# Optimization experiments

Measured on AMD Instinct MI355X. Metric: run time of the kernel, lower is better.

The kernel has to match this reference:

```python
import jax, jax.numpy as jnp
import numpy as np

NPOINT = 512
RADIUS = 0.2
NSAMPLE = 32
BN_EPS = 1e-5


def setup_inputs() -> dict:
    key = jax.random.key(0)
    ks = jax.random.split(key, 8)
    B, N, C = 8, 16384, 64
    xyz = jax.random.uniform(ks[0], (B, N, 3), dtype=jnp.float32)
    features = jax.random.normal(ks[1], (B, N, C), dtype=jnp.float32)
    # shared-MLP 1x1 conv weights (out, in), BN params per layer
    w0 = jax.random.normal(ks[2], (64, 67), dtype=jnp.float32) * 0.1
    w1 = jax.random.normal(ks[3], (64, 64), dtype=jnp.float32) * 0.1
    w2 = jax.random.normal(ks[4], (128, 64), dtype=jnp.float32) * 0.1
    return dict(
        xyz=xyz, features=features,
        w0=w0, g0=jnp.ones((64,)), b0=jnp.zeros((64,)), m0=jnp.zeros((64,)), v0=jnp.ones((64,)),
        w1=w1, g1=jnp.ones((64,)), b1=jnp.zeros((64,)), m1=jnp.zeros((64,)), v1=jnp.ones((64,)),
        w2=w2, g2=jnp.ones((128,)), b2=jnp.zeros((128,)), m2=jnp.zeros((128,)), v2=jnp.ones((128,)),
    )


def furthest_point_sample(xyz, npoint):
    # xyz: (B, N, 3) -> idx: (B, npoint) int32. Sequential farthest-point selection.
    B, N, _ = xyz.shape
    binds = jnp.arange(B)

    def step(carry, _):
        dists, last = carry  # (B,N), (B,)
        p = xyz[binds, last]                      # (B, 3)
        d = jnp.sum((xyz - p[:, None, :]) ** 2, axis=-1)  # (B, N)
        dists = jnp.minimum(dists, d)
        nxt = jnp.argmax(dists, axis=-1).astype(jnp.int32)
        return (dists, nxt), last

    init = (jnp.full((B, N), jnp.inf, dtype=xyz.dtype), jnp.zeros((B,), jnp.int32))
    _, idx = jax.lax.scan(step, init, None, length=npoint)  # (npoint, B)
    return idx.T  # (B, npoint)


def ball_query(xyz, new_xyz, radius, nsample):
    # xyz: (B,N,3), new_xyz: (B,S,3) -> idx (B,S,nsample) int32
    N = xyz.shape[1]
    d2 = jnp.sum((new_xyz[:, :, None, :] - xyz[:, None, :, :]) ** 2, axis=-1)  # (B,S,N)
    cand = jnp.where(d2 <= radius * radius, jnp.arange(N, dtype=jnp.int32), N)
    cand = jnp.sort(cand, axis=-1)[..., :nsample]  # first nsample in-radius indices
    first = cand[..., :1]
    idx = jnp.where(cand == N, first, cand)       # duplicate first hit when short
    return jnp.minimum(idx, N - 1)


def _mlp_layer(x, w, g, b, m, v):
    # x: (B,S,K,Cin); 1x1 conv + BN(inference) + ReLU
    h = jnp.einsum('bskc,oc->bsko', x, w)
    h = (h - m) * (g * jax.lax.rsqrt(v + BN_EPS)) + b
    return jax.nn.relu(h)


def reference(xyz, features, w0, g0, b0, m0, v0, w1, g1, b1, m1, v1, w2, g2, b2, m2, v2):
    B = xyz.shape[0]
    binds = jnp.arange(B)[:, None, None]
    fps_idx = furthest_point_sample(xyz, NPOINT)                # (B, S)
    new_xyz = jnp.take_along_axis(xyz, fps_idx[..., None], axis=1)  # (B, S, 3)
    idx = ball_query(xyz, new_xyz, RADIUS, NSAMPLE)             # (B, S, K)
    grouped_xyz = xyz[binds, idx] - new_xyz[:, :, None, :]      # (B,S,K,3) centered
    grouped_feat = features[binds, idx]                         # (B,S,K,C)
    x = jnp.concatenate([grouped_xyz, grouped_feat], axis=-1)   # (B,S,K,3+C)
    x = _mlp_layer(x, w0, g0, b0, m0, v0)
    x = _mlp_layer(x, w1, g1, b1, m1, v1)
    x = _mlp_layer(x, w2, g2, b2, m2, v2)                       # (B,S,K,128)
    new_features = jnp.max(x, axis=2)                           # max-pool over nsample
    new_features = jnp.transpose(new_features, (0, 2, 1))       # (B, 128, S) channel-first
    return new_xyz, new_features
```

## Files before the change

kernel.cpp:

```cpp
#include <hip/hip_runtime.h>
#include <hip/hip_bf16.h>

#define NPT   16384
#define NQ    512
#define NS    32
#define BATCH 8

typedef float f32x2 __attribute__((ext_vector_type(2)));

template <int CTRL>
__device__ inline double dpp_f64(double x)
{
    const unsigned long long u = (unsigned long long)__double_as_longlong(x);
    int lo = (int)(unsigned)u;
    int hi = (int)(unsigned)(u >> 32);
    lo = __builtin_amdgcn_update_dpp(0, lo, CTRL, 0xf, 0xf, true);
    hi = __builtin_amdgcn_update_dpp(0, hi, CTRL, 0xf, 0xf, true);
    return __longlong_as_double(
        (long long)(((unsigned long long)(unsigned)hi << 32) | (unsigned)lo));
}

__global__ __launch_bounds__(512)
__attribute__((amdgpu_waves_per_eu(2, 2)))
void fps_kernel(const float* __restrict__ xyz, float* __restrict__ new_xyz)
{
#pragma clang fp contract(off)
    const int b = blockIdx.x;
    const int t = threadIdx.x;
    const float* xb = xyz + (size_t)b * NPT * 3;

    f32x2 xr[16], yr[16], zr[16], dr[16];
    const float INF = __int_as_float(0x7f800000);
#pragma unroll
    for (int j = 0; j < 16; ++j) {
        const int p0 = (2 * j) * 512 + t;
        const int p1 = (2 * j + 1) * 512 + t;
        xr[j] = (f32x2){xb[p0 * 3 + 0], xb[p1 * 3 + 0]};
        yr[j] = (f32x2){xb[p0 * 3 + 1], xb[p1 * 3 + 1]};
        zr[j] = (f32x2){xb[p0 * 3 + 2], xb[p1 * 3 + 2]};
        dr[j] = (f32x2){INF, INF};
    }

    __shared__ unsigned long long red[2][8];

    float px = xb[0], py = xb[1], pz = xb[2];

    for (int s = 0; s < NQ; ++s) {
        if (t == 0) {
            float* o = new_xyz + ((size_t)b * NQ + s) * 3;
            o[0] = px; o[1] = py; o[2] = pz;
        }
        if (s == NQ - 1) break;

        const f32x2 pxv = {px, px}, pyv = {py, py}, pzv = {pz, pz};
        float dmax = -1.0f;
        int   bi_  = 0;
#pragma unroll
        for (int j = 0; j < 16; ++j) {
            const f32x2 dx = xr[j] - pxv;
            const f32x2 dy = yr[j] - pyv;
            const f32x2 dz = zr[j] - pzv;
            f32x2 d = (dx * dx + dy * dy);
            d = d + dz * dz;
            const f32x2 dn = __builtin_elementwise_min(dr[j], d);
            dr[j] = dn;
            const float ds = (dn.x >= dn.y) ? dn.x : dn.y;
            const int   is = (dn.x >= dn.y) ? (2 * j) : (2 * j + 1);
            if (ds > dmax) { dmax = ds; bi_ = is; }
        }

        const unsigned pidx = (unsigned)(bi_ * 512 + t);
        double kd = __longlong_as_double((long long)(
            ((unsigned long long)__float_as_uint(dmax) << 32) | (unsigned)(~pidx)));

        kd = fmax(kd, dpp_f64<0x111>(kd));
        kd = fmax(kd, dpp_f64<0x112>(kd));
        kd = fmax(kd, dpp_f64<0x114>(kd));
        kd = fmax(kd, dpp_f64<0x118>(kd));
        kd = fmax(kd, dpp_f64<0x142>(kd));
        kd = fmax(kd, dpp_f64<0x143>(kd));

        if ((t & 63) == 63)
            red[s & 1][t >> 6] = (unsigned long long)__double_as_longlong(kd);
        __syncthreads();

        double kc = __longlong_as_double((long long)red[s & 1][t & 7]);
        kc = fmax(kc, dpp_f64<0x111>(kc));
        kc = fmax(kc, dpp_f64<0x112>(kc));
        kc = fmax(kc, dpp_f64<0x114>(kc));

        const unsigned long long kw = (unsigned long long)__double_as_longlong(kc);
        const unsigned lo7 = (unsigned)__builtin_amdgcn_readlane((int)(unsigned)kw, 7);
        const int nxt = (int)(unsigned)(~lo7);

        px = xb[nxt * 3 + 0];
        py = xb[nxt * 3 + 1];
        pz = xb[nxt * 3 + 2];
    }
}

__global__ __launch_bounds__(256) void bq_kernel(const float* __restrict__ xyz,
                                                 const float* __restrict__ newxyz,
                                                 int* __restrict__ gidx)
{
    const int wid  = (blockIdx.x * 256 + threadIdx.x) >> 6;
    const int lane = threadIdx.x & 63;
    const int b    = wid >> 9;
    const float* xb = xyz + (size_t)b * NPT * 3;

    const float qx = newxyz[wid * 3 + 0];
    const float qy = newxyz[wid * 3 + 1];
    const float qz = newxyz[wid * 3 + 2];
    int* out = gidx + (size_t)wid * NS;

    const float R2 = 0.04f;
    int cnt = 0, first = -1;

    for (int base = 0; base < NPT; base += 64) {
        const int p = base + lane;
        const float dx = __fsub_rn(xb[p * 3 + 0], qx);
        const float dy = __fsub_rn(xb[p * 3 + 1], qy);
        const float dz = __fsub_rn(xb[p * 3 + 2], qz);
        const float d  = __fadd_rn(__fadd_rn(__fmul_rn(dx, dx), __fmul_rn(dy, dy)),
                                   __fmul_rn(dz, dz));
        const bool in = (d <= R2);
        const unsigned long long m = __ballot(in);
        if (first < 0 && m) first = base + (__ffsll((unsigned long long)m) - 1);
        if (in) {
            const int pos = cnt + __popcll(m & ((1ull << lane) - 1ull));
            if (pos < NS) out[pos] = p;
        }
        cnt += __popcll(m);
        if (cnt >= NS) break;
    }
    if (cnt < NS) {
        const int f = (cnt > 0) ? first : (NPT - 1);
        for (int j = cnt + lane; j < NS; j += 64) out[j] = f;
    }
}

template <int OP>
__device__ inline void mlp_layer(const float* __restrict__ inb,
                                 const float* __restrict__ wbuf,
                                 const float* __restrict__ scp,
                                 const float* __restrict__ bip,
                                 float* __restrict__ outb, int nchunk, int t)
{
    const int ko = t & 15;
    const int og = t >> 4;
    const int o0 = og * OP;
    float acc0[OP], acc1[OP];
#pragma unroll
    for (int j = 0; j < OP; ++j) { acc0[j] = 0.f; acc1[j] = 0.f; }

    for (int cc = 0; cc < nchunk; ++cc) {
        const int c = cc * 4;
        const float4 xa = *(const float4*)(inb + ko * 68 + c);
        const float4 xb = *(const float4*)(inb + (ko + 16) * 68 + c);
#pragma unroll
        for (int j = 0; j < OP; ++j) {
            const float4 w = *(const float4*)(wbuf + (o0 + j) * 68 + c);
            acc0[j] += xa.x * w.x + xa.y * w.y + xa.z * w.z + xa.w * w.w;
            acc1[j] += xb.x * w.x + xb.y * w.y + xb.z * w.z + xb.w * w.w;
        }
    }
#pragma unroll
    for (int j = 0; j < OP; ++j) {
        const float sv = scp[o0 + j], bv = bip[o0 + j];
        acc0[j] = fmaxf(acc0[j] * sv + bv, 0.f);
        acc1[j] = fmaxf(acc1[j] * sv + bv, 0.f);
    }
#pragma unroll
    for (int jb = 0; jb < OP; jb += 4) {
        *(float4*)(outb + ko * 68 + o0 + jb) =
            make_float4(acc0[jb], acc0[jb + 1], acc0[jb + 2], acc0[jb + 3]);
        *(float4*)(outb + (ko + 16) * 68 + o0 + jb) =
            make_float4(acc1[jb], acc1[jb + 1], acc1[jb + 2], acc1[jb + 3]);
    }
}

__device__ inline void mlp_layer2(const float* __restrict__ inb,
                                  const float* __restrict__ wbuf,
                                  const float* __restrict__ scp,
                                  const float* __restrict__ bip,
                                  float* __restrict__ out, int b, int s, int t)
{
    const int ko = t & 15;
    const int og = t >> 4;
    const int o0 = og * 8;
    float acc0[8], acc1[8];
#pragma unroll
    for (int j = 0; j < 8; ++j) { acc0[j] = 0.f; acc1[j] = 0.f; }

    for (int cc = 0; cc < 16; ++cc) {
        const int c = cc * 4;
        const float4 xa = *(const float4*)(inb + ko * 68 + c);
        const float4 xb = *(const float4*)(inb + (ko + 16) * 68 + c);
#pragma unroll
        for (int j = 0; j < 8; ++j) {
            const float4 w = *(const float4*)(wbuf + (o0 + j) * 68 + c);
            acc0[j] += xa.x * w.x + xa.y * w.y + xa.z * w.z + xa.w * w.w;
            acc1[j] += xb.x * w.x + xb.y * w.y + xb.z * w.z + xb.w * w.w;
        }
    }
    float v[8];
#pragma unroll
    for (int j = 0; j < 8; ++j) {
        const float sv = scp[o0 + j], bv = bip[o0 + j];
        const float h0 = fmaxf(acc0[j] * sv + bv, 0.f);
        const float h1 = fmaxf(acc1[j] * sv + bv, 0.f);
        v[j] = fmaxf(h0, h1);
    }
#pragma unroll
    for (int m = 1; m <= 8; m <<= 1) {
#pragma unroll
        for (int j = 0; j < 8; ++j) v[j] = fmaxf(v[j], __shfl_xor(v[j], m, 64));
    }
    if (ko == 0) {
#pragma unroll
        for (int j = 0; j < 8; ++j)
            out[((size_t)b * 128 + o0 + j) * NQ + s] = v[j];
    }
}

__global__ __launch_bounds__(256) void mlp_kernel(
    const float* __restrict__ xyz, const float* __restrict__ feat,
    const float* __restrict__ newxyz, const int* __restrict__ gidx,
    const float* __restrict__ w0, const float* __restrict__ g0,
    const float* __restrict__ b0, const float* __restrict__ m0,
    const float* __restrict__ v0,
    const float* __restrict__ w1, const float* __restrict__ g1,
    const float* __restrict__ b1, const float* __restrict__ m1,
    const float* __restrict__ v1,
    const float* __restrict__ w2, const float* __restrict__ g2,
    const float* __restrict__ b2, const float* __restrict__ m2,
    const float* __restrict__ v2,
    float* __restrict__ out)
{
    __shared__ float wbuf[128 * 68];
    __shared__ float bufA[32 * 68];
    __shared__ float bufB[32 * 68];
    __shared__ float sc[256], bi[256];

    const int t   = threadIdx.x;
    const int grp = blockIdx.x;
    const int b   = grp >> 9;
    const int s   = grp & (NQ - 1);
    const int* gi = gidx + (size_t)grp * NS;

    float4 r1[4], r2[8];
    {
        const float4* s1 = (const float4*)(w1 + t * 16);
#pragma unroll
        for (int q = 0; q < 4; ++q) r1[q] = s1[q];
        const float4* s2 = (const float4*)(w2 + t * 32);
#pragma unroll
        for (int q = 0; q < 8; ++q) r2[q] = s2[q];
    }

    if (t < 64) {
        const float sv = g0[t] * rsqrtf(v0[t] + 1e-5f);
        sc[t] = sv; bi[t] = b0[t] - m0[t] * sv;
    } else if (t < 128) {
        const int j = t - 64;
        const float sv = g1[j] * rsqrtf(v1[j] + 1e-5f);
        sc[t] = sv; bi[t] = b1[j] - m1[j] * sv;
    } else {
        const int j = t - 128;
        const float sv = g2[j] * rsqrtf(v2[j] + 1e-5f);
        sc[t] = sv; bi[t] = b2[j] - m2[j] * sv;
    }

    for (int i = t; i < 64 * 68; i += 256) {
        const int o = i / 68, c = i - o * 68;
        float v;
        if (c < 64)       v = w0[o * 67 + 3 + c];
        else if (c < 67)  v = w0[o * 67 + (c - 64)];
        else              v = 0.f;
        wbuf[i] = v;
    }

    {
        const int k = t >> 3, f = t & 7;
        const int p = gi[k];
        const float* fr = feat + ((size_t)b * NPT + p) * 64 + f * 8;
        const float4 a0 = *(const float4*)fr;
        const float4 a1 = *(const float4*)(fr + 4);
        *(float4*)(bufA + k * 68 + f * 8)     = a0;
        *(float4*)(bufA + k * 68 + f * 8 + 4) = a1;
        if (f == 0) {
            const float qx = newxyz[grp * 3 + 0];
            const float qy = newxyz[grp * 3 + 1];
            const float qz = newxyz[grp * 3 + 2];
            const float* xp = xyz + ((size_t)b * NPT + p) * 3;
            bufA[k * 68 + 64] = xp[0] - qx;
            bufA[k * 68 + 65] = xp[1] - qy;
            bufA[k * 68 + 66] = xp[2] - qz;
            bufA[k * 68 + 67] = 0.f;
        }
    }
    __syncthreads();

    mlp_layer<4>(bufA, wbuf, sc, bi, bufB, 17, t);
    __syncthreads();

    {
        float* dst = wbuf + (t >> 2) * 68 + (t & 3) * 16;
#pragma unroll
        for (int q = 0; q < 4; ++q) *(float4*)(dst + 4 * q) = r1[q];
    }
    __syncthreads();

    mlp_layer<4>(bufB, wbuf, sc + 64, bi + 64, bufA, 16, t);
    __syncthreads();

    {
        float* dst = wbuf + (t >> 1) * 68 + (t & 1) * 32;
#pragma unroll
        for (int q = 0; q < 8; ++q) *(float4*)(dst + 4 * q) = r2[q];
    }
    __syncthreads();

    mlp_layer2(bufA, wbuf, sc + 128, bi + 128, out, b, s, t);
}

extern "C" void kernel_launch(void* const* d_in, const int* in_sizes, int n_in,
                              void* d_out, int out_size, void* d_ws, size_t ws_size,
                              hipStream_t stream)
{
    const float* xyz  = (const float*)d_in[0];
    const float* feat = (const float*)d_in[1];
    const float* w0 = (const float*)d_in[2];
    const float* g0 = (const float*)d_in[3];
    const float* b0 = (const float*)d_in[4];
    const float* m0 = (const float*)d_in[5];
    const float* v0 = (const float*)d_in[6];
    const float* w1 = (const float*)d_in[7];
    const float* g1 = (const float*)d_in[8];
    const float* b1 = (const float*)d_in[9];
    const float* m1 = (const float*)d_in[10];
    const float* v1 = (const float*)d_in[11];
    const float* w2 = (const float*)d_in[12];
    const float* g2 = (const float*)d_in[13];
    const float* b2 = (const float*)d_in[14];
    const float* m2 = (const float*)d_in[15];
    const float* v2 = (const float*)d_in[16];

    float* out      = (float*)d_out;
    float* new_xyz  = out;
    float* out_feat = out + BATCH * NQ * 3;
    int*   gidx     = (int*)d_ws;

    fps_kernel<<<BATCH, 512, 0, stream>>>(xyz, new_xyz);
    bq_kernel<<<(BATCH * NQ * 64) / 256, 256, 0, stream>>>(xyz, new_xyz, gidx);
    mlp_kernel<<<BATCH * NQ, 256, 0, stream>>>(xyz, feat, new_xyz, gidx,
                                               w0, g0, b0, m0, v0,
                                               w1, g1, b1, m1, v1,
                                               w2, g2, b2, m2, v2,
                                               out_feat);
}
```

Measured before the change: 1.109 ms.

## Halve MLP weight LDS buffer, split last layer in two passes, reorder block mapping

The last MLP layer now runs in two 64-output halves that share a single 64x68 weight buffer, which cuts shared memory per block by about 17 KB so more blocks can be resident per CU. The neighbour feature gather loads are issued at kernel start, ahead of the weight staging, to overlap global latency. Block indices are interleaved across batches, likely to spread accesses. The cost is an extra barrier and a second weight-staging pass in the final layer.

Measured after the change: 1.227 ms. 10.6% more time.

```diff
diff --git a/kernel.cpp b/kernel.cpp
--- a/kernel.cpp
+++ b/kernel.cpp
@@ -179,47 +179,22 @@
     }
 }
 
-__device__ inline void mlp_layer2(const float* __restrict__ inb,
+__device__ inline void mlp_l2_acc(const float* __restrict__ inb,
                                   const float* __restrict__ wbuf,
-                                  const float* __restrict__ scp,
-                                  const float* __restrict__ bip,
-                                  float* __restrict__ out, int b, int s, int t)
+                                  float acc0[4], float acc1[4], int t)
 {
     const int ko = t & 15;
-    const int og = t >> 4;
-    const int o0 = og * 8;
-    float acc0[8], acc1[8];
-#pragma unroll
-    for (int j = 0; j < 8; ++j) { acc0[j] = 0.f; acc1[j] = 0.f; }
-
+    const int o0 = (t >> 4) * 4;
     for (int cc = 0; cc < 16; ++cc) {
         const int c = cc * 4;
         const float4 xa = *(const float4*)(inb + ko * 68 + c);
         const float4 xb = *(const float4*)(inb + (ko + 16) * 68 + c);
 #pragma unroll
-        for (int j = 0; j < 8; ++j) {
+        for (int j = 0; j < 4; ++j) {
             const float4 w = *(const float4*)(wbuf + (o0 + j) * 68 + c);
             acc0[j] += xa.x * w.x + xa.y * w.y + xa.z * w.z + xa.w * w.w;
             acc1[j] += xb.x * w.x + xb.y * w.y + xb.z * w.z + xb.w * w.w;
         }
-    }
-    float v[8];
-#pragma unroll
-    for (int j = 0; j < 8; ++j) {
-        const float sv = scp[o0 + j], bv = bip[o0 + j];
-        const float h0 = fmaxf(acc0[j] * sv + bv, 0.f);
-        const float h1 = fmaxf(acc1[j] * sv + bv, 0.f);
-        v[j] = fmaxf(h0, h1);
-    }
-#pragma unroll
-    for (int m = 1; m <= 8; m <<= 1) {
-#pragma unroll
-        for (int j = 0; j < 8; ++j) v[j] = fmaxf(v[j], __shfl_xor(v[j], m, 64));
-    }
-    if (ko == 0) {
-#pragma unroll
-        for (int j = 0; j < 8; ++j)
-            out[((size_t)b * 128 + o0 + j) * NQ + s] = v[j];
     }
 }
 
@@ -237,16 +212,32 @@
     const float* __restrict__ v2,
     float* __restrict__ out)
 {
-    __shared__ float wbuf[128 * 68];
+    __shared__ float wbuf[64 * 68];
     __shared__ float bufA[32 * 68];
     __shared__ float bufB[32 * 68];
     __shared__ float sc[256], bi[256];
 
-    const int t   = threadIdx.x;
-    const int grp = blockIdx.x;
+    const int t = threadIdx.x;
+    const int grp = ((blockIdx.x & 7) << 9) | (blockIdx.x >> 3);
     const int b   = grp >> 9;
     const int s   = grp & (NQ - 1);
     const int* gi = gidx + (size_t)grp * NS;
+
+    const int k = t >> 3, f = t & 7;
+    const int p = gi[k];
+    const float* fr = feat + ((size_t)b * NPT + p) * 64 + f * 8;
+    const float4 a0 = *(const float4*)fr;
+    const float4 a1 = *(const float4*)(fr + 4);
+    float c64 = 0.f, c65 = 0.f, c66 = 0.f;
+    if (f == 0) {
+        const float qx = newxyz[grp * 3 + 0];
+        const float qy = newxyz[grp * 3 + 1];
+        const float qz = newxyz[grp * 3 + 2];
+        const float* xp = xyz + ((size_t)b * NPT + p) * 3;
+        c64 = xp[0] - qx;
+        c65 = xp[1] - qy;
+        c66 = xp[2] - qz;
+    }
 
     float4 r1[4], r2[8];
     {
@@ -280,24 +271,13 @@
         wbuf[i] = v;
     }
 
-    {
-        const int k = t >> 3, f = t & 7;
-        const int p = gi[k];
-        const float* fr = feat + ((size_t)b * NPT + p) * 64 + f * 8;
-        const float4 a0 = *(const float4*)fr;
-        const float4 a1 = *(const float4*)(fr + 4);
-        *(float4*)(bufA + k * 68 + f * 8)     = a0;
-        *(float4*)(bufA + k * 68 + f * 8 + 4) = a1;
-        if (f == 0) {
-            const float qx = newxyz[grp * 3 + 0];
-            const float qy = newxyz[grp * 3 + 1];
-            const float qz = newxyz[grp * 3 + 2];
-            const float* xp = xyz + ((size_t)b * NPT + p) * 3;
-            bufA[k * 68 + 64] = xp[0] - qx;
-            bufA[k * 68 + 65] = xp[1] - qy;
-            bufA[k * 68 + 66] = xp[2] - qz;
-            bufA[k * 68 + 67] = 0.f;
-        }
+    *(float4*)(bufA + k * 68 + f * 8)     = a0;
+    *(float4*)(bufA + k * 68 + f * 8 + 4) = a1;
+    if (f == 0) {
+        bufA[k * 68 + 64] = c64;
+        bufA[k * 68 + 65] = c65;
+        bufA[k * 68 + 66] = c66;
+        bufA[k * 68 + 67] = 0.f;
     }
     __syncthreads();
 
@@ -314,14 +294,55 @@
     mlp_layer<4>(bufB, wbuf, sc + 64, bi + 64, bufA, 16, t);
     __syncthreads();
 
-    {
+    if (t < 128) {
         float* dst = wbuf + (t >> 1) * 68 + (t & 1) * 32;
 #pragma unroll
         for (int q = 0; q < 8; ++q) *(float4*)(dst + 4 * q) = r2[q];
     }
     __syncthreads();
 
-    mlp_layer2(bufA, wbuf, sc + 128, bi + 128, out, b, s, t);
+    float accA0[4] = {0.f, 0.f, 0.f, 0.f}, accA1[4] = {0.f, 0.f, 0.f, 0.f};
+    mlp_l2_acc(bufA, wbuf, accA0, accA1, t);
+    __syncthreads();
+
+    if (t >= 128) {
+        float* dst = wbuf + ((t >> 1) - 64) * 68 + (t & 1) * 32;
+#pragma unroll
+        for (int q = 0; q < 8; ++q) *(float4*)(dst + 4 * q) = r2[q];
+    }
+    __syncthreads();
+
+    float accB0[4] = {0.f, 0.f, 0.f, 0.f}, accB1[4] = {0.f, 0.f, 0.f, 0.f};
+    mlp_l2_acc(bufA, wbuf, accB0, accB1, t);
+
+    const int ko = t & 15;
+    const int o4 = (t >> 4) * 4;
+    const float* scp = sc + 128;
+    const float* bip = bi + 128;
+    float v[8];
+#pragma unroll
+    for (int j = 0; j < 4; ++j) {
+        const float svA = scp[o4 + j],      bvA = bip[o4 + j];
+        const float svB = scp[64 + o4 + j], bvB = bip[64 + o4 + j];
+        const float hA0 = fmaxf(accA0[j] * svA + bvA, 0.f);
+        const float hA1 = fmaxf(accA1[j] * svA + bvA, 0.f);
+        const float hB0 = fmaxf(accB0[j] * svB + bvB, 0.f);
+        const float hB1 = fmaxf(accB1[j] * svB + bvB, 0.f);
+        v[j]     = fmaxf(hA0, hA1);
+        v[4 + j] = fmaxf(hB0, hB1);
+    }
+#pragma unroll
+    for (int m = 1; m <= 8; m <<= 1) {
+#pragma unroll
+        for (int j = 0; j < 8; ++j) v[j] = fmaxf(v[j], __shfl_xor(v[j], m, 64));
+    }
+    if (ko == 0) {
+#pragma unroll
+        for (int j = 0; j < 4; ++j) {
+            out[((size_t)b * 128 + o4 + j) * NQ + s]      = v[j];
+            out[((size_t)b * 128 + 64 + o4 + j) * NQ + s] = v[4 + j];
+        }
+    }
 }
 
 extern "C" void kernel_launch(void* const* d_in, const int* in_sizes, int n_in,
```

## Split FPS across four cooperating blocks per batch with global atomic barrier

Applied to the files above, without the earlier changes.

Farthest point sampling for each batch is spread over four workgroups, each holding a quarter of the points in registers. The per-step argmax is combined through a global buffer, an atomic counter and a spin-wait. The goal is more CUs working on the sequential FPS loop and less per-thread work per step. The cost is a device-scope round trip and spin on every one of the 512 steps, and correctness depends on all 32 blocks being resident at the same time. The workspace region used for the counters overlaps the gidx buffer, which is only written later by bq_kernel.

Measured after the change: 1.796 ms. 62.0% more time.

```diff
diff --git a/kernel.cpp b/kernel.cpp
--- a/kernel.cpp
+++ b/kernel.cpp
@@ -5,6 +5,7 @@
 #define NQ    512
 #define NS    32
 #define BATCH 8
+#define FPB   4
 
 typedef float f32x2 __attribute__((ext_vector_type(2)));
 
@@ -21,20 +22,24 @@
 }
 
 __global__ __launch_bounds__(512)
-__attribute__((amdgpu_waves_per_eu(2, 2)))
-void fps_kernel(const float* __restrict__ xyz, float* __restrict__ new_xyz)
+void fps_kernel(const float* __restrict__ xyz, float* __restrict__ new_xyz,
+                unsigned long long* __restrict__ kbuf,
+                unsigned* __restrict__ cnt)
 {
 #pragma clang fp contract(off)
-    const int b = blockIdx.x;
-    const int t = threadIdx.x;
+    const int bb  = blockIdx.x;
+    const int b   = bb >> 2;
+    const int blk = bb & 3;
+    const int t   = threadIdx.x;
     const float* xb = xyz + (size_t)b * NPT * 3;
-
-    f32x2 xr[16], yr[16], zr[16], dr[16];
+    const int pbase = blk * (NPT / FPB);
+
+    f32x2 xr[4], yr[4], zr[4], dr[4];
     const float INF = __int_as_float(0x7f800000);
 #pragma unroll
-    for (int j = 0; j < 16; ++j) {
-        const int p0 = (2 * j) * 512 + t;
-        const int p1 = (2 * j + 1) * 512 + t;
+    for (int j = 0; j < 4; ++j) {
+        const int p0 = pbase + (2 * j) * 512 + t;
+        const int p1 = pbase + (2 * j + 1) * 512 + t;
         xr[j] = (f32x2){xb[p0 * 3 + 0], xb[p1 * 3 + 0]};
         yr[j] = (f32x2){xb[p0 * 3 + 1], xb[p1 * 3 + 1]};
         zr[j] = (f32x2){xb[p0 * 3 + 2], xb[p1 * 3 + 2]};
@@ -42,11 +47,12 @@
     }
 
     __shared__ unsigned long long red[2][8];
+    __shared__ int nxt_s;
 
     float px = xb[0], py = xb[1], pz = xb[2];
 
     for (int s = 0; s < NQ; ++s) {
-        if (t == 0) {
+        if (blk == 0 && t == 0) {
             float* o = new_xyz + ((size_t)b * NQ + s) * 3;
             o[0] = px; o[1] = py; o[2] = pz;
         }
@@ -56,7 +62,7 @@
         float dmax = -1.0f;
         int   bi_  = 0;
 #pragma unroll
-        for (int j = 0; j < 16; ++j) {
+        for (int j = 0; j < 4; ++j) {
             const f32x2 dx = xr[j] - pxv;
             const f32x2 dy = yr[j] - pyv;
             const f32x2 dz = zr[j] - pzv;
@@ -69,7 +75,7 @@
             if (ds > dmax) { dmax = ds; bi_ = is; }
         }
 
-        const unsigned pidx = (unsigned)(bi_ * 512 + t);
+        const unsigned pidx = (unsigned)(pbase + bi_ * 512 + t);
         double kd = __longlong_as_double((long long)(
             ((unsigned long long)__float_as_uint(dmax) << 32) | (unsigned)(~pidx)));
 
@@ -91,7 +97,33 @@
 
         const unsigned long long kw = (unsigned long long)__double_as_longlong(kc);
         const unsigned lo7 = (unsigned)__builtin_amdgcn_readlane((int)(unsigned)kw, 7);
-        const int nxt = (int)(unsigned)(~lo7);
+        const unsigned hi7 = (unsigned)__builtin_amdgcn_readlane((int)(unsigned)(kw >> 32), 7);
+        const unsigned long long kblock = ((unsigned long long)hi7 << 32) | lo7;
+
+        if (t == 0) {
+            __hip_atomic_store(&kbuf[(s & 1) * (BATCH * FPB) + bb], kblock,
+                               __ATOMIC_RELAXED, __HIP_MEMORY_SCOPE_AGENT);
+            __hip_atomic_fetch_add(&cnt[b], 1u,
+                                   __ATOMIC_RELEASE, __HIP_MEMORY_SCOPE_AGENT);
+            const unsigned tgt = (unsigned)(FPB * (s + 1));
+            while (__hip_atomic_load(&cnt[b], __ATOMIC_ACQUIRE,
+                                     __HIP_MEMORY_SCOPE_AGENT) < tgt)
+                __builtin_amdgcn_s_sleep(1);
+            const unsigned long long* kb4 =
+                kbuf + (s & 1) * (BATCH * FPB) + b * FPB;
+            unsigned long long w = __hip_atomic_load(&kb4[0], __ATOMIC_RELAXED,
+                                                     __HIP_MEMORY_SCOPE_AGENT);
+#pragma unroll
+            for (int q = 1; q < FPB; ++q) {
+                const unsigned long long v =
+                    __hip_atomic_load(&kb4[q], __ATOMIC_RELAXED,
+                                      __HIP_MEMORY_SCOPE_AGENT);
+                if (v > w) w = v;
+            }
+            nxt_s = (int)(unsigned)(~(unsigned)w);
+        }
+        __syncthreads();
+        const int nxt = nxt_s;
 
         px = xb[nxt * 3 + 0];
         py = xb[nxt * 3 + 1];
@@ -351,7 +383,11 @@
     float* out_feat = out + BATCH * NQ * 3;
     int*   gidx     = (int*)d_ws;
 
-    fps_kernel<<<BATCH, 512, 0, stream>>>(xyz, new_xyz);
+    unsigned long long* kbuf = (unsigned long long*)d_ws;
+    unsigned* cnt = (unsigned*)((char*)d_ws + 1024);
+    hipMemsetAsync(d_ws, 0, 2048, stream);
+
+    fps_kernel<<<BATCH * FPB, 512, 0, stream>>>(xyz, new_xyz, kbuf, cnt);
     bq_kernel<<<(BATCH * NQ * 64) / 256, 256, 0, stream>>>(xyz, new_xyz, gidx);
     mlp_kernel<<<BATCH * NQ, 256, 0, stream>>>(xyz, feat, new_xyz, gidx,
                                                w0, g0, b0, m0, v0,
```

## Fuse FPS, ball query and MLP into one persistent producer-consumer kernel

Applied to the files above, without the earlier changes.

Merges the three kernels into a single persistent launch: 8 blocks run furthest point sampling and publish each new centroid with a release flag per batch. The other 248 blocks poll those flags and run ball query plus the three-layer MLP for two queries at a time, so grouping and MLP overlap with the serial FPS loop. This removes the separate launches and the global index buffer, but adds spin-waiting, a memset, and a reliance on producer and consumer blocks being co-resident. It also reloads weights for every query pair.

Result: slower. 1.700 ms (+53.3%).

```diff
diff --git a/kernel.cpp b/kernel.cpp
--- a/kernel.cpp
+++ b/kernel.cpp
@@ -5,6 +5,8 @@
 #define NQ    512
 #define NS    32
 #define BATCH 8
+#define NCONS 248
+#define NPAIR 2048
 
 typedef float f32x2 __attribute__((ext_vector_type(2)));
 
@@ -20,125 +22,6 @@
         (long long)(((unsigned long long)(unsigned)hi << 32) | (unsigned)lo));
 }
 
-__global__ __launch_bounds__(512)
-__attribute__((amdgpu_waves_per_eu(2, 2)))
-void fps_kernel(const float* __restrict__ xyz, float* __restrict__ new_xyz)
-{
-#pragma clang fp contract(off)
-    const int b = blockIdx.x;
-    const int t = threadIdx.x;
-    const float* xb = xyz + (size_t)b * NPT * 3;
-
-    f32x2 xr[16], yr[16], zr[16], dr[16];
-    const float INF = __int_as_float(0x7f800000);
-#pragma unroll
-    for (int j = 0; j < 16; ++j) {
-        const int p0 = (2 * j) * 512 + t;
-        const int p1 = (2 * j + 1) * 512 + t;
-        xr[j] = (f32x2){xb[p0 * 3 + 0], xb[p1 * 3 + 0]};
-        yr[j] = (f32x2){xb[p0 * 3 + 1], xb[p1 * 3 + 1]};
-        zr[j] = (f32x2){xb[p0 * 3 + 2], xb[p1 * 3 + 2]};
-        dr[j] = (f32x2){INF, INF};
-    }
-
-    __shared__ unsigned long long red[2][8];
-
-    float px = xb[0], py = xb[1], pz = xb[2];
-
-    for (int s = 0; s < NQ; ++s) {
-        if (t == 0) {
-            float* o = new_xyz + ((size_t)b * NQ + s) * 3;
-            o[0] = px; o[1] = py; o[2] = pz;
-        }
-        if (s == NQ - 1) break;
-
-        const f32x2 pxv = {px, px}, pyv = {py, py}, pzv = {pz, pz};
-        float dmax = -1.0f;
-        int   bi_  = 0;
-#pragma unroll
-        for (int j = 0; j < 16; ++j) {
-            const f32x2 dx = xr[j] - pxv;
-            const f32x2 dy = yr[j] - pyv;
-            const f32x2 dz = zr[j] - pzv;
-            f32x2 d = (dx * dx + dy * dy);
-            d = d + dz * dz;
-            const f32x2 dn = __builtin_elementwise_min(dr[j], d);
-            dr[j] = dn;
-            const float ds = (dn.x >= dn.y) ? dn.x : dn.y;
-            const int   is = (dn.x >= dn.y) ? (2 * j) : (2 * j + 1);
-            if (ds > dmax) { dmax = ds; bi_ = is; }
-        }
-
-        const unsigned pidx = (unsigned)(bi_ * 512 + t);
-        double kd = __longlong_as_double((long long)(
-            ((unsigned long long)__float_as_uint(dmax) << 32) | (unsigned)(~pidx)));
-
-        kd = fmax(kd, dpp_f64<0x111>(kd));
-        kd = fmax(kd, dpp_f64<0x112>(kd));
-        kd = fmax(kd, dpp_f64<0x114>(kd));
-        kd = fmax(kd, dpp_f64<0x118>(kd));
-        kd = fmax(kd, dpp_f64<0x142>(kd));
-        kd = fmax(kd, dpp_f64<0x143>(kd));
-
-        if ((t & 63) == 63)
-            red[s & 1][t >> 6] = (unsigned long long)__double_as_longlong(kd);
-        __syncthreads();
-
-        double kc = __longlong_as_double((long long)red[s & 1][t & 7]);
-        kc = fmax(kc, dpp_f64<0x111>(kc));
-        kc = fmax(kc, dpp_f64<0x112>(kc));
-        kc = fmax(kc, dpp_f64<0x114>(kc));
-
-        const unsigned long long kw = (unsigned long long)__double_as_longlong(kc);
-        const unsigned lo7 = (unsigned)__builtin_amdgcn_readlane((int)(unsigned)kw, 7);
-        const int nxt = (int)(unsigned)(~lo7);
-
-        px = xb[nxt * 3 + 0];
-        py = xb[nxt * 3 + 1];
-        pz = xb[nxt * 3 + 2];
-    }
-}
-
-__global__ __launch_bounds__(256) void bq_kernel(const float* __restrict__ xyz,
-                                                 const float* __restrict__ newxyz,
-                                                 int* __restrict__ gidx)
-{
-    const int wid  = (blockIdx.x * 256 + threadIdx.x) >> 6;
-    const int lane = threadIdx.x & 63;
-    const int b    = wid >> 9;
-    const float* xb = xyz + (size_t)b * NPT * 3;
-
-    const float qx = newxyz[wid * 3 + 0];
-    const float qy = newxyz[wid * 3 + 1];
-    const float qz = newxyz[wid * 3 + 2];
-    int* out = gidx + (size_t)wid * NS;
-
-    const float R2 = 0.04f;
-    int cnt = 0, first = -1;
-
-    for (int base = 0; base < NPT; base += 64) {
-        const int p = base + lane;
-        const float dx = __fsub_rn(xb[p * 3 + 0], qx);
-        const float dy = __fsub_rn(xb[p * 3 + 1], qy);
-        const float dz = __fsub_rn(xb[p * 3 + 2], qz);
-        const float d  = __fadd_rn(__fadd_rn(__fmul_rn(dx, dx), __fmul_rn(dy, dy)),
-                                   __fmul_rn(dz, dz));
-        const bool in = (d <= R2);
-        const unsigned long long m = __ballot(in);
-        if (first < 0 && m) first = base + (__ffsll((unsigned long long)m) - 1);
-        if (in) {
-            const int pos = cnt + __popcll(m & ((1ull << lane) - 1ull));
-            if (pos < NS) out[pos] = p;
-        }
-        cnt += __popcll(m);
-        if (cnt >= NS) break;
-    }
-    if (cnt < NS) {
-        const int f = (cnt > 0) ? first : (NPT - 1);
-        for (int j = cnt + lane; j < NS; j += 64) out[j] = f;
-    }
-}
-
 template <int OP>
 __device__ inline void mlp_layer(const float* __restrict__ inb,
                                  const float* __restrict__ wbuf,
@@ -223,105 +106,256 @@
     }
 }
 
-__global__ __launch_bounds__(256) void mlp_kernel(
-    const float* __restrict__ xyz, const float* __restrict__ feat,
-    const float* __restrict__ newxyz, const int* __restrict__ gidx,
-    const float* __restrict__ w0, const float* __restrict__ g0,
-    const float* __restrict__ b0, const float* __restrict__ m0,
-    const float* __restrict__ v0,
-    const float* __restrict__ w1, const float* __restrict__ g1,
-    const float* __restrict__ b1, const float* __restrict__ m1,
-    const float* __restrict__ v1,
-    const float* __restrict__ w2, const float* __restrict__ g2,
-    const float* __restrict__ b2, const float* __restrict__ m2,
-    const float* __restrict__ v2,
-    float* __restrict__ out)
+__global__ __launch_bounds__(512)
+void fused_kernel(const float* __restrict__ xyz, const float* __restrict__ feat,
+                  float* __restrict__ new_xyz,
+                  const float* __restrict__ w0, const float* __restrict__ g0,
+                  const float* __restrict__ b0, const float* __restrict__ m0,
+                  const float* __restrict__ v0,
+                  const float* __restrict__ w1, const float* __restrict__ g1,
+                  const float* __restrict__ b1, const float* __restrict__ m1,
+                  const float* __restrict__ v1,
+                  const float* __restrict__ w2, const float* __restrict__ g2,
+                  const float* __restrict__ b2, const float* __restrict__ m2,
+                  const float* __restrict__ v2,
+                  float* __restrict__ out, unsigned* __restrict__ flags)
 {
     __shared__ float wbuf[128 * 68];
-    __shared__ float bufA[32 * 68];
-    __shared__ float bufB[32 * 68];
+    __shared__ float bufA[2][32 * 68];
+    __shared__ float bufB[2][32 * 68];
     __shared__ float sc[256], bi[256];
-
-    const int t   = threadIdx.x;
-    const int grp = blockIdx.x;
-    const int b   = grp >> 9;
-    const int s   = grp & (NQ - 1);
-    const int* gi = gidx + (size_t)grp * NS;
-
-    float4 r1[4], r2[8];
-    {
-        const float4* s1 = (const float4*)(w1 + t * 16);
-#pragma unroll
-        for (int q = 0; q < 4; ++q) r1[q] = s1[q];
-        const float4* s2 = (const float4*)(w2 + t * 32);
-#pragma unroll
-        for (int q = 0; q < 8; ++q) r2[q] = s2[q];
-    }
-
-    if (t < 64) {
-        const float sv = g0[t] * rsqrtf(v0[t] + 1e-5f);
-        sc[t] = sv; bi[t] = b0[t] - m0[t] * sv;
-    } else if (t < 128) {
-        const int j = t - 64;
-        const float sv = g1[j] * rsqrtf(v1[j] + 1e-5f);
-        sc[t] = sv; bi[t] = b1[j] - m1[j] * sv;
-    } else {
-        const int j = t - 128;
-        const float sv = g2[j] * rsqrtf(v2[j] + 1e-5f);
-        sc[t] = sv; bi[t] = b2[j] - m2[j] * sv;
-    }
-
-    for (int i = t; i < 64 * 68; i += 256) {
-        const int o = i / 68, c = i - o * 68;
-        float v;
-        if (c < 64)       v = w0[o * 67 + 3 + c];
-        else if (c < 67)  v = w0[o * 67 + (c - 64)];
-        else              v = 0.f;
-        wbuf[i] = v;
-    }
-
-    {
-        const int k = t >> 3, f = t & 7;
-        const int p = gi[k];
-        const float* fr = feat + ((size_t)b * NPT + p) * 64 + f * 8;
-        const float4 a0 = *(const float4*)fr;
-        const float4 a1 = *(const float4*)(fr + 4);
-        *(float4*)(bufA + k * 68 + f * 8)     = a0;
-        *(float4*)(bufA + k * 68 + f * 8 + 4) = a1;
-        if (f == 0) {
-            const float qx = newxyz[grp * 3 + 0];
-            const float qy = newxyz[grp * 3 + 1];
-            const float qz = newxyz[grp * 3 + 2];
-            const float* xp = xyz + ((size_t)b * NPT + p) * 3;
-            bufA[k * 68 + 64] = xp[0] - qx;
-            bufA[k * 68 + 65] = xp[1] - qy;
-            bufA[k * 68 + 66] = xp[2] - qz;
-            bufA[k * 68 + 67] = 0.f;
-        }
-    }
-    __syncthreads();
-
-    mlp_layer<4>(bufA, wbuf, sc, bi, bufB, 17, t);
-    __syncthreads();
-
-    {
-        float* dst = wbuf + (t >> 2) * 68 + (t & 3) * 16;
-#pragma unroll
-        for (int q = 0; q < 4; ++q) *(float4*)(dst + 4 * q) = r1[q];
-    }
-    __syncthreads();
-
-    mlp_layer<4>(bufB, wbuf, sc + 64, bi + 64, bufA, 16, t);
-    __syncthreads();
-
-    {
-        float* dst = wbuf + (t >> 1) * 68 + (t & 1) * 32;
-#pragma unroll
-        for (int q = 0; q < 8; ++q) *(float4*)(dst + 4 * q) = r2[q];
-    }
-    __syncthreads();
-
-    mlp_layer2(bufA, wbuf, sc + 128, bi + 128, out, b, s, t);
+    __shared__ int   gidxL[2][NS];
+    __shared__ float qbuf[2][3];
+    __shared__ unsigned long long red[2][8];
+
+    const int t = threadIdx.x;
+
+    if (blockIdx.x < BATCH) {
+#pragma clang fp contract(off)
+        __builtin_amdgcn_s_setprio(3);
+        const int b = blockIdx.x;
+        const float* xb = xyz + (size_t)b * NPT * 3;
+
+        f32x2 xr[16], yr[16], zr[16], dr[16];
+        const float INF = __int_as_float(0x7f800000);
+#pragma unroll
+        for (int j = 0; j < 16; ++j) {
+            const int p0 = (2 * j) * 512 + t;
+            const int p1 = (2 * j + 1) * 512 + t;
+            xr[j] = (f32x2){xb[p0 * 3 + 0], xb[p1 * 3 + 0]};
+            yr[j] = (f32x2){xb[p0 * 3 + 1], xb[p1 * 3 + 1]};
+            zr[j] = (f32x2){xb[p0 * 3 + 2], xb[p1 * 3 + 2]};
+            dr[j] = (f32x2){INF, INF};
+        }
+
+        float px = xb[0], py = xb[1], pz = xb[2];
+
+        for (int s = 0; s < NQ; ++s) {
+            if (t == 0) {
+                unsigned* o = (unsigned*)(new_xyz + ((size_t)b * NQ + s) * 3);
+                __hip_atomic_store(o + 0, __float_as_uint(px),
+                                   __ATOMIC_RELAXED, __HIP_MEMORY_SCOPE_AGENT);
+                __hip_atomic_store(o + 1, __float_as_uint(py),
+                                   __ATOMIC_RELAXED, __HIP_MEMORY_SCOPE_AGENT);
+                __hip_atomic_store(o + 2, __float_as_uint(pz),
+                                   __ATOMIC_RELAXED, __HIP_MEMORY_SCOPE_AGENT);
+                __hip_atomic_store(&flags[b * 32], (unsigned)(s + 1),
+                                   __ATOMIC_RELEASE, __HIP_MEMORY_SCOPE_AGENT);
+            }
+            if (s == NQ - 1) break;
+
+            const f32x2 pxv = {px, px}, pyv = {py, py}, pzv = {pz, pz};
+            float dmax = -1.0f;
+            int   bi_  = 0;
+#pragma unroll
+            for (int j = 0; j < 16; ++j) {
+                const f32x2 dx = xr[j] - pxv;
+                const f32x2 dy = yr[j] - pyv;
+                const f32x2 dz = zr[j] - pzv;
+                f32x2 d = (dx * dx + dy * dy);
+                d = d + dz * dz;
+                const f32x2 dn = __builtin_elementwise_min(dr[j], d);
+                dr[j] = dn;
+                const float ds = (dn.x >= dn.y) ? dn.x : dn.y;
+                const int   is = (dn.x >= dn.y) ? (2 * j) : (2 * j + 1);
+                if (ds > dmax) { dmax = ds; bi_ = is; }
+            }
+
+            const unsigned pidx = (unsigned)(bi_ * 512 + t);
+            double kd = __longlong_as_double((long long)(
+                ((unsigned long long)__float_as_uint(dmax) << 32) |
+                (unsigned)(~pidx)));
+
+            kd = fmax(kd, dpp_f64<0x111>(kd));
+            kd = fmax(kd, dpp_f64<0x112>(kd));
+            kd = fmax(kd, dpp_f64<0x114>(kd));
+            kd = fmax(kd, dpp_f64<0x118>(kd));
+            kd = fmax(kd, dpp_f64<0x142>(kd));
+            kd = fmax(kd, dpp_f64<0x143>(kd));
+
+            if ((t & 63) == 63)
+                red[s & 1][t >> 6] = (unsigned long long)__double_as_longlong(kd);
+            __syncthreads();
+
+            double kc = __longlong_as_double((long long)red[s & 1][t & 7]);
+            kc = fmax(kc, dpp_f64<0x111>(kc));
+            kc = fmax(kc, dpp_f64<0x112>(kc));
+            kc = fmax(kc, dpp_f64<0x114>(kc));
+
+            const unsigned long long kw =
+                (unsigned long long)__double_as_longlong(kc);
+            const unsigned lo7 =
+                (unsigned)__builtin_amdgcn_readlane((int)(unsigned)kw, 7);
+            const int nxt = (int)(unsigned)(~lo7);
+
+            px = xb[nxt * 3 + 0];
+            py = xb[nxt * 3 + 1];
+            pz = xb[nxt * 3 + 2];
+        }
+        return;
+    }
+
+    const int h  = t >> 8;
+    const int tt = t & 255;
+    const int cb = blockIdx.x - BATCH;
+
+    if (t < 256) {
+        if (tt < 64) {
+            const float sv = g0[tt] * rsqrtf(v0[tt] + 1e-5f);
+            sc[tt] = sv; bi[tt] = b0[tt] - m0[tt] * sv;
+        } else if (tt < 128) {
+            const int j = tt - 64;
+            const float sv = g1[j] * rsqrtf(v1[j] + 1e-5f);
+            sc[tt] = sv; bi[tt] = b1[j] - m1[j] * sv;
+        } else {
+            const int j = tt - 128;
+            const float sv = g2[j] * rsqrtf(v2[j] + 1e-5f);
+            sc[tt] = sv; bi[tt] = b2[j] - m2[j] * sv;
+        }
+    }
+
+    for (int pair = cb; pair < NPAIR; pair += NCONS) {
+        const int idx = pair * 2;
+        const int s   = idx >> 3;
+        const int bA  = idx & 7;
+        const int bh  = bA + h;
+
+        if (t == 0) {
+            while (__hip_atomic_load(&flags[bA * 32], __ATOMIC_ACQUIRE,
+                                     __HIP_MEMORY_SCOPE_AGENT) <= (unsigned)s)
+                __builtin_amdgcn_s_sleep(16);
+            while (__hip_atomic_load(&flags[(bA + 1) * 32], __ATOMIC_ACQUIRE,
+                                     __HIP_MEMORY_SCOPE_AGENT) <= (unsigned)s)
+                __builtin_amdgcn_s_sleep(16);
+        }
+        __syncthreads();
+
+        if (tt < 64) {
+            const int lane = tt;
+            const float* xb = xyz + (size_t)bh * NPT * 3;
+            float qx = 0.f, qy = 0.f, qz = 0.f;
+            if (lane == 0) {
+                const unsigned* q =
+                    (const unsigned*)(new_xyz + ((size_t)bh * NQ + s) * 3);
+                qx = __uint_as_float(__hip_atomic_load(q + 0, __ATOMIC_RELAXED,
+                                                       __HIP_MEMORY_SCOPE_AGENT));
+                qy = __uint_as_float(__hip_atomic_load(q + 1, __ATOMIC_RELAXED,
+                                                       __HIP_MEMORY_SCOPE_AGENT));
+                qz = __uint_as_float(__hip_atomic_load(q + 2, __ATOMIC_RELAXED,
+                                                       __HIP_MEMORY_SCOPE_AGENT));
+                qbuf[h][0] = qx; qbuf[h][1] = qy; qbuf[h][2] = qz;
+            }
+            qx = __shfl(qx, 0, 64); qy = __shfl(qy, 0, 64); qz = __shfl(qz, 0, 64);
+
+            int* outg = gidxL[h];
+            const float R2 = 0.04f;
+            int cnt = 0, first = -1;
+            for (int base = 0; base < NPT; base += 64) {
+                const int p = base + lane;
+                const float dx = __fsub_rn(xb[p * 3 + 0], qx);
+                const float dy = __fsub_rn(xb[p * 3 + 1], qy);
+                const float dz = __fsub_rn(xb[p * 3 + 2], qz);
+                const float d  = __fadd_rn(__fadd_rn(__fmul_rn(dx, dx),
+                                                     __fmul_rn(dy, dy)),
+                                           __fmul_rn(dz, dz));
+                const bool in = (d <= R2);
+                const unsigned long long m = __ballot(in);
+                if (first < 0 && m) first = base + (__ffsll((unsigned long long)m) - 1);
+                if (in) {
+                    const int pos = cnt + __popcll(m & ((1ull << lane) - 1ull));
+                    if (pos < NS) outg[pos] = p;
+                }
+                cnt += __popcll(m);
+                if (cnt >= NS) break;
+            }
+            if (cnt < NS) {
+                const int f2 = (cnt > 0) ? first : (NPT - 1);
+                for (int j = cnt + lane; j < NS; j += 64) outg[j] = f2;
+            }
+        }
+        __syncthreads();
+
+        float4 r1[4], r2[8];
+        if (t < 256) {
+            const float4* s1 = (const float4*)(w1 + tt * 16);
+#pragma unroll
+            for (int q = 0; q < 4; ++q) r1[q] = s1[q];
+            const float4* s2 = (const float4*)(w2 + tt * 32);
+#pragma unroll
+            for (int q = 0; q < 8; ++q) r2[q] = s2[q];
+
+            for (int i = tt; i < 64 * 68; i += 256) {
+                const int o = i / 68, c = i - o * 68;
+                float v;
+                if (c < 64)       v = w0[o * 67 + 3 + c];
+                else if (c < 67)  v = w0[o * 67 + (c - 64)];
+                else              v = 0.f;
+                wbuf[i] = v;
+            }
+        }
+
+        {
+            const int k = tt >> 3, f = tt & 7;
+            const int p = gidxL[h][k];
+            const float* fr = feat + ((size_t)bh * NPT + p) * 64 + f * 8;
+            const float4 a0 = *(const float4*)fr;
+            const float4 a1 = *(const float4*)(fr + 4);
+            float* bA_ = bufA[h];
+            *(float4*)(bA_ + k * 68 + f * 8)     = a0;
+            *(float4*)(bA_ + k * 68 + f * 8 + 4) = a1;
+            if (f == 0) {
+                const float* xp = xyz + ((size_t)bh * NPT + p) * 3;
+                bA_[k * 68 + 64] = xp[0] - qbuf[h][0];
+                bA_[k * 68 + 65] = xp[1] - qbuf[h][1];
+                bA_[k * 68 + 66] = xp[2] - qbuf[h][2];
+                bA_[k * 68 + 67] = 0.f;
+            }
+        }
+        __syncthreads();
+
+        mlp_layer<4>(bufA[h], wbuf, sc, bi, bufB[h], 17, tt);
+        __syncthreads();
+
+        if (t < 256) {
+            float* dst = wbuf + (tt >> 2) * 68 + (tt & 3) * 16;
+#pragma unroll
+            for (int q = 0; q < 4; ++q) *(float4*)(dst + 4 * q) = r1[q];
+        }
+        __syncthreads();
+
+        mlp_layer<4>(bufB[h], wbuf, sc + 64, bi + 64, bufA[h], 16, tt);
+        __syncthreads();
+
+        if (t < 256) {
+            float* dst = wbuf + (tt >> 1) * 68 + (tt & 1) * 32;
+#pragma unroll
+            for (int q = 0; q < 8; ++q) *(float4*)(dst + 4 * q) = r2[q];
+        }
+        __syncthreads();
+
+        mlp_layer2(bufA[h], wbuf, sc + 128, bi + 128, out, bh, s, tt);
+        __syncthreads();
+    }
 }
 
 extern "C" void kernel_launch(void* const* d_in, const int* in_sizes, int n_in,
@@ -349,13 +383,14 @@
     float* out      = (float*)d_out;
     float* new_xyz  = out;
     float* out_feat = out + BATCH * NQ * 3;
-    int*   gidx     = (int*)d_ws;
-
-    fps_kernel<<<BATCH, 512, 0, stream>>>(xyz, new_xyz);
-    bq_kernel<<<(BATCH * NQ * 64) / 256, 256, 0, stream>>>(xyz, new_xyz, gidx);
-    mlp_kernel<<<BATCH * NQ, 256, 0, stream>>>(xyz, feat, new_xyz, gidx,
-                                               w0, g0, b0, m0, v0,
-                                               w1, g1, b1, m1, v1,
-                                               w2, g2, b2, m2, v2,
-                                               out_feat);
-}
+
+    unsigned* flags = (unsigned*)d_ws;
+    (void)hipMemsetAsync(d_ws, 0, 1024, stream);
+
+    fused_kernel<<<BATCH + NCONS, 512, 0, stream>>>(
+        xyz, feat, new_xyz,
+        w0, g0, b0, m0, v0,
+        w1, g1, b1, m1, v1,
+        w2, g2, b2, m2, v2,
+        out_feat, flags);
+}
```
